# Performance work log

Measured on AMD Instinct MI355X. Metric: run time of the kernel, lower is better.

The kernel has to match this reference:

```python
import jax, jax.numpy as jnp
import numpy as np

B, N, E, H = 2, 2048, 1024, 16
D = E // H


def setup_inputs() -> dict:
    key = jax.random.key(0)
    ks = jax.random.split(key, 10)
    s = 0.02  # small init so softmax is well-conditioned
    return {
        "x": jax.random.normal(ks[0], (B, N, E), jnp.float32),
        "y": jax.random.normal(ks[1], (B, N, E), jnp.float32),
        # W stored as [in, out]; torch Linear computes x @ W_t.T + b, equivalent here.
        "Wq": jax.random.normal(ks[2], (E, E), jnp.float32) * s,
        "bq": jax.random.normal(ks[3], (E,), jnp.float32) * s,
        "Wk": jax.random.normal(ks[4], (E, E), jnp.float32) * s,
        "bk": jax.random.normal(ks[5], (E,), jnp.float32) * s,
        "Wv": jax.random.normal(ks[6], (E, E), jnp.float32) * s,
        "bv": jax.random.normal(ks[7], (E,), jnp.float32) * s,
        "Wo": jax.random.normal(ks[8], (E, E), jnp.float32) * s,
        "bo": jax.random.normal(ks[9], (E,), jnp.float32) * s,
    }


def _split_heads(t):
    # [b, n, (h d)] -> [b, h, n, d]
    b, n, e = t.shape
    return t.reshape(b, n, H, D).transpose(0, 2, 1, 3)


def reference(x, y, Wq, bq, Wk, bk, Wv, bv, Wo, bo):
    q = _split_heads(x @ Wq + bq)          # [b,h,n,d]
    k = _split_heads(y @ Wk + bk)
    v = _split_heads(y @ Wv + bv)
    energy = jnp.einsum('bhqd,bhkd->bhqk', q, k)            # [b,h,n,n]
    # Faithful quirk: softmax first, then divide by sqrt(emb_size).
    scaling = jnp.asarray(E, x.dtype) ** 0.5
    att = jax.nn.softmax(energy, axis=-1) / scaling
    out = jnp.einsum('bhqk,bhkd->bhqd', att, v)             # [b,h,n,d]
    out = out.transpose(0, 2, 1, 3).reshape(x.shape[0], x.shape[1], E)
    return out @ Wo + bo
```

## Files before the change

### kernel.cpp

```cpp
#include <hip/hip_runtime.h>
#include <stdint.h>

#define BATCH 2
#define SEQ   2048
#define EMB   1024
#define NH    16
#define HD    64
#define MROWS (BATCH*SEQ)
#define LOG2E 1.4426950408889634f

using bf16x8 = __attribute__((ext_vector_type(8))) short;
using f32x4  = __attribute__((ext_vector_type(4))) float;
using f32x16 = __attribute__((ext_vector_type(16))) float;

__device__ __forceinline__ unsigned short f2bf(float f) {
  __bf16 b = (__bf16)f;
  return __builtin_bit_cast(unsigned short, b);
}

__device__ __forceinline__ unsigned int cvtpk_bf16(float lo, float hi) {
  unsigned int w;
  asm("v_cvt_pk_bf16_f32 %0, %1, %2" : "=v"(w) : "v"(lo), "v"(hi));
  return w;
}

#if __has_builtin(__builtin_amdgcn_exp2f)
__device__ __forceinline__ float fast_exp2(float x) { return __builtin_amdgcn_exp2f(x); }
#else
__device__ __forceinline__ float fast_exp2(float x) {
  float r;
  asm("v_exp_f32 %0, %1\n\ts_nop 1" : "=v"(r) : "v"(x));
  return r;
}
#endif

__device__ __forceinline__ void swap32(unsigned int& a, unsigned int& b, int hi) {
#if __has_builtin(__builtin_amdgcn_permlane32_swap)
  (void)hi;
  typedef unsigned int u32x2_t __attribute__((ext_vector_type(2)));
  u32x2_t r = __builtin_amdgcn_permlane32_swap(a, b, false, false);
  a = r[0]; b = r[1];
#else
  const unsigned int ca = __shfl_xor(a, 32), cb = __shfl_xor(b, 32);
  const unsigned int na = hi ? cb : a;
  const unsigned int nb = hi ? b : ca;
  a = na; b = nb;
#endif
}

__device__ __forceinline__ float xadd32(float x, int hi) {
  unsigned int a = __builtin_bit_cast(unsigned int, x), b = a;
  swap32(a, b, hi);
  return __builtin_bit_cast(float, a) + __builtin_bit_cast(float, b);
}

__device__ __forceinline__ void async_load16(const void* g, void* l) {
  __builtin_amdgcn_global_load_lds(
      (__attribute__((address_space(1))) void*)g,
      (__attribute__((address_space(3))) void*)l,
      16, 0, 0);
}

__global__ __launch_bounds__(256) void prep_kernel(
    const float* __restrict__ x, const float* __restrict__ y,
    const float* __restrict__ Wq, const float* __restrict__ Wk,
    const float* __restrict__ Wv, const float* __restrict__ Wo,
    unsigned short* __restrict__ xb, unsigned short* __restrict__ yb,
    unsigned short* __restrict__ WtAll) {
  __shared__ unsigned short tile[64][65];
  const int lin = blockIdx.x;
  if (lin < 8192) {
    const float* in = (lin < 4096) ? x : y;
    unsigned short* out = (lin < 4096) ? xb : yb;
    const int i = (lin & 4095) * 256 + threadIdx.x;
    const float4 v = reinterpret_cast<const float4*>(in)[i];
    ushort4 o;
    o.x = f2bf(v.x); o.y = f2bf(v.y); o.z = f2bf(v.z); o.w = f2bf(v.w);
    reinterpret_cast<ushort4*>(out)[i] = o;
    return;
  }
  const int tw = lin - 8192;
  const int z = tw >> 8;
  const float* W = (z == 0) ? Wq : (z == 1) ? Wk : (z == 2) ? Wv : Wo;
  unsigned short* Wt = WtAll + (size_t)z * EMB * EMB;
  const int tc = threadIdx.x & 15;
  const int tr = threadIdx.x >> 4;
  const int n0 = ((tw >> 4) & 15) * 64, k0 = (tw & 15) * 64;
#pragma unroll
  for (int rr = 0; rr < 4; ++rr) {
    const int row = rr * 16 + tr;
    float4 v = *reinterpret_cast<const float4*>(W + (size_t)(k0 + row) * EMB + n0 + tc * 4);
    tile[tc * 4 + 0][row] = f2bf(v.x);
    tile[tc * 4 + 1][row] = f2bf(v.y);
    tile[tc * 4 + 2][row] = f2bf(v.z);
    tile[tc * 4 + 3][row] = f2bf(v.w);
  }
  __syncthreads();
#pragma unroll
  for (int rr = 0; rr < 4; ++rr) {
    const int row = rr * 16 + tr;
    ushort4 o;
    o.x = tile[row][tc * 4 + 0];
    o.y = tile[row][tc * 4 + 1];
    o.z = tile[row][tc * 4 + 2];
    o.w = tile[row][tc * 4 + 3];
    *reinterpret_cast<ushort4*>(Wt + (size_t)(n0 + row) * EMB + k0 + tc * 4) = o;
  }
}

#define BN 128
#define BK 32
#define NKS (EMB/BK)

template <int BMt>
__global__ __launch_bounds__(256, 3) void gemm_kernel(
    const unsigned short* __restrict__ xb,
    const unsigned short* __restrict__ yb,
    const unsigned short* __restrict__ attnb,
    const unsigned short* __restrict__ WtAll,
    const float* __restrict__ bq, const float* __restrict__ bk,
    const float* __restrict__ bv, const float* __restrict__ bo,
    unsigned short* __restrict__ Qb, unsigned short* __restrict__ Kb,
    unsigned short* __restrict__ Vt, float* __restrict__ dout,
    int phase) {
  __shared__ __align__(16) unsigned short As[3][BMt * BK];
  __shared__ __align__(16) unsigned short Bs[3][BN * BK];

  const int z = blockIdx.z;
  const unsigned short* A;
  const unsigned short* Bt;
  const float* bias;
  int mode;
  if (phase == 0) {
    A    = (z == 0) ? xb : yb;
    Bt   = WtAll + (size_t)z * EMB * EMB;
    bias = (z == 0) ? bq : (z == 1) ? bk : bv;
    mode = z;
  } else {
    A = attnb; Bt = WtAll + (size_t)3 * EMB * EMB; bias = bo; mode = 3;
  }

  const int tid = threadIdx.x;
  const int lane = tid & 63, wid = tid >> 6;
  constexpr int WC  = (BMt == 128) ? 2 : 4;
  constexpr int WCW = 128 / WC;
  constexpr int JN  = WCW / 16;
  const int wr = (BMt == 128) ? (wid >> 1) : 0;
  const int wc = (BMt == 128) ? (wid & 1) : wid;
  const int l15 = lane & 15, l4 = lane >> 4;
  const int m0 = blockIdx.y * BMt, n0 = blockIdx.x * BN;

  const int crow = tid >> 2;
  const int cslot = tid & 3;
  const int ssw = cslot ^ ((crow >> 1) & 3);
  const int rsw = (l15 >> 1) & 3;

  auto GSTAGE = [&](int b, int kt) {
    if constexpr (BMt == 128) {
#pragma unroll
      for (int it = 0; it < 2; ++it)
        async_load16(A + (size_t)(m0 + it * 64 + crow) * EMB + kt + ssw * 8,
                     (char*)As[b] + it * 4096 + wid * 1024);
    } else {
      async_load16(A + (size_t)(m0 + crow) * EMB + kt + ssw * 8,
                   (char*)As[b] + wid * 1024);
    }
#pragma unroll
    for (int it = 0; it < 2; ++it)
      async_load16(Bt + (size_t)(n0 + it * 64 + crow) * EMB + kt + ssw * 8,
                   (char*)Bs[b] + it * 4096 + wid * 1024);
  };

  GSTAGE(0, 0);
  GSTAGE(1, BK);

  f32x4 acc[4][JN] = {};

  int buf = 0, sb = 2;
  for (int s = 0; s < NKS; ++s) {
    __builtin_amdgcn_sched_barrier(0);
    if (s < NKS - 1) {
      if constexpr (BMt == 128) {
        asm volatile("s_waitcnt vmcnt(4)" ::: "memory");
      } else {
        asm volatile("s_waitcnt vmcnt(3)" ::: "memory");
      }
    } else {
      asm volatile("s_waitcnt vmcnt(0)" ::: "memory");
    }
    __builtin_amdgcn_s_barrier();
    __builtin_amdgcn_sched_barrier(0);

    if (s + 2 < NKS) { GSTAGE(sb, (s + 2) * BK); }

    bf16x8 af[4], bfr[JN];
#pragma unroll
    for (int i = 0; i < 4; ++i)
      af[i] = *reinterpret_cast<const bf16x8*>(
          (const char*)As[buf] + (wr * 64 + i * 16 + l15) * 64 + ((l4 ^ rsw) * 16));
#pragma unroll
    for (int j = 0; j < JN; ++j)
      bfr[j] = *reinterpret_cast<const bf16x8*>(
          (const char*)Bs[buf] + (wc * WCW + j * 16 + l15) * 64 + ((l4 ^ rsw) * 16));
#pragma unroll
    for (int i = 0; i < 4; ++i)
#pragma unroll
      for (int j = 0; j < JN; ++j)
        acc[i][j] = __builtin_amdgcn_mfma_f32_16x16x32_bf16(af[i], bfr[j], acc[i][j], 0, 0, 0);

    buf = (buf == 2) ? 0 : buf + 1;
    sb  = (sb  == 2) ? 0 : sb + 1;
  }

#pragma unroll
  for (int i = 0; i < 4; ++i) {
#pragma unroll
    for (int j = 0; j < JN; ++j) {
      const int col = n0 + wc * WCW + j * 16 + l15;
      const float bsv = bias[col];
#pragma unroll
      for (int r = 0; r < 4; ++r) {
        const int row = m0 + wr * 64 + i * 16 + l4 * 4 + r;
        const float v = acc[i][j][r] + bsv;
        if (mode == 3) {
          dout[(size_t)row * EMB + col] = v;
        } else {
          const int b = row >> 11, n = row & (SEQ - 1);
          const int h = col >> 6, d = col & (HD - 1);
          if (mode == 0)
            Qb[(((size_t)(b * NH + h)) * SEQ + n) * HD + d] = f2bf(v);
          else if (mode == 1)
            Kb[(((size_t)(b * NH + h)) * SEQ + n) * HD + d] = f2bf(v * LOG2E);
          else
            Vt[(((size_t)(b * NH + h)) * HD + d) * SEQ + n] = f2bf(v);
        }
      }
    }
  }
}

#define KVB 64
#define NT  (SEQ/KVB)

__global__ __launch_bounds__(256, 2) void flash_kernel(
    const unsigned short* __restrict__ Qb,
    const unsigned short* __restrict__ Kb,
    const unsigned short* __restrict__ Vt,
    unsigned short* __restrict__ attnb) {
  __shared__ __align__(16) char Ks[3][8192];
  __shared__ __align__(16) char Vs[3][8192];

  const int tid = threadIdx.x;
  const int lane = tid & 63, wid = tid >> 6;
  const int l31 = lane & 31, hi = lane >> 5;

  const int lin = blockIdx.x;
  const int swz = (lin & 7) * 64 + (lin >> 3);
  const int bh = swz >> 4;
  const int qt = swz & 15;
  const int bb = bh >> 4, hh = bh & 15;
  const int q0 = qt * 128 + wid * 32;

  const unsigned short* Qp = Qb + (size_t)bh * SEQ * HD;
  const unsigned short* Kp = Kb + (size_t)bh * SEQ * HD;
  const unsigned short* Vp = Vt + (size_t)bh * HD * SEQ;

  const int srow = tid >> 3;
  const int sslot = tid & 7;

  bf16x8 qf[4];
#pragma unroll
  for (int kt = 0; kt < 4; ++kt)
    qf[kt] = *reinterpret_cast<const bf16x8*>(Qp + (size_t)(q0 + l31) * HD + kt * 16 + hi * 8);

#define SWZ(r) (((r) & 7) ^ (((r) >> 3) & 7))
#define STAGE(b, kv)                                                          \
  {                                                                           \
    _Pragma("unroll")                                                         \
    for (int it = 0; it < 2; ++it) {                                          \
      const int r = it * 32 + srow;                                           \
      async_load16(Kp + (size_t)((kv) + r) * HD + ((sslot ^ SWZ(r)) * 8),     \
                   Ks[b] + it * 4096 + tid * 16);                             \
      async_load16(Vp + (size_t)r * SEQ + (kv) + ((sslot ^ SWZ(r)) * 8),      \
                   Vs[b] + it * 4096 + tid * 16);                             \
    }                                                                         \
  }

  STAGE(0, 0)
  STAGE(1, KVB)

  f32x16 accO[2] = {};
  float lp[8] = {0.f, 0.f, 0.f, 0.f, 0.f, 0.f, 0.f, 0.f};

  int buf = 0, sb = 2;
  for (int t = 0; t < NT; ++t) {
    __builtin_amdgcn_sched_barrier(0);
    if (t < NT - 1) {
      asm volatile("s_waitcnt vmcnt(4)" ::: "memory");
    } else {
      asm volatile("s_waitcnt vmcnt(0)" ::: "memory");
    }
    __builtin_amdgcn_s_barrier();
    __builtin_amdgcn_sched_barrier(0);

    if (t + 2 < NT) { STAGE(sb, (t + 2) * KVB) }

    bf16x8 kf[2][4];
#pragma unroll
    for (int t2 = 0; t2 < 2; ++t2)
#pragma unroll
      for (int kt = 0; kt < 4; ++kt) {
        const int key = t2 * 32 + l31;
        kf[t2][kt] = *reinterpret_cast<const bf16x8*>(
            Ks[buf] + key * 128 + (((kt * 2 + hi) ^ SWZ(key)) * 16));
      }
    bf16x8 vf[2][4];
#pragma unroll
    for (int dt = 0; dt < 2; ++dt)
#pragma unroll
      for (int kt = 0; kt < 4; ++kt) {
        const int d = dt * 32 + l31;
        vf[dt][kt] = *reinterpret_cast<const bf16x8*>(
            Vs[buf] + d * 128 + (((kt * 2 + hi) ^ SWZ(d)) * 16));
      }

    f32x16 sc[2] = {};
#pragma unroll
    for (int t2 = 0; t2 < 2; ++t2)
#pragma unroll
      for (int kt = 0; kt < 4; ++kt)
        sc[t2] = __builtin_amdgcn_mfma_f32_32x32x16_bf16(kf[t2][kt], qf[kt], sc[t2], 0, 0, 0);

#pragma unroll
    for (int t2 = 0; t2 < 2; ++t2)
#pragma unroll
      for (int r = 0; r < 16; ++r) {
        sc[t2][r] = fast_exp2(sc[t2][r]);
        lp[(t2 << 2) | (r & 3)] += sc[t2][r];
      }

    bf16x8 pf[4];
#pragma unroll
    for (int kt = 0; kt < 4; ++kt) {
      const int t2 = kt >> 1, g = (kt & 1) * 8;
      unsigned int Aw = cvtpk_bf16(sc[t2][g + 0], sc[t2][g + 1]);
      unsigned int Cw = cvtpk_bf16(sc[t2][g + 2], sc[t2][g + 3]);
      unsigned int Bw = cvtpk_bf16(sc[t2][g + 4], sc[t2][g + 5]);
      unsigned int Dw = cvtpk_bf16(sc[t2][g + 6], sc[t2][g + 7]);
      swap32(Aw, Bw, hi);
      swap32(Cw, Dw, hi);
      union { unsigned int u[4]; bf16x8 v; } cvt;
      cvt.u[0] = Aw; cvt.u[1] = Cw; cvt.u[2] = Bw; cvt.u[3] = Dw;
      pf[kt] = cvt.v;
    }

#pragma unroll
    for (int dt = 0; dt < 2; ++dt)
#pragma unroll
      for (int kt = 0; kt < 4; ++kt)
        accO[dt] = __builtin_amdgcn_mfma_f32_32x32x16_bf16(vf[dt][kt], pf[kt], accO[dt], 0, 0, 0);

    buf = (buf == 2) ? 0 : buf + 1;
    sb  = (sb  == 2) ? 0 : sb + 1;
  }
#undef STAGE
#undef SWZ

  const float ls = ((lp[0] + lp[1]) + (lp[2] + lp[3])) +
                   ((lp[4] + lp[5]) + (lp[6] + lp[7]));
  const float lI = xadd32(ls, hi);
  const float inv = 1.0f / (lI * 32.0f);
  const size_t obase = ((size_t)(bb * SEQ + q0 + l31)) * EMB + hh * HD;
#pragma unroll
  for (int dt = 0; dt < 2; ++dt)
#pragma unroll
    for (int rr = 0; rr < 4; ++rr) {
      ushort4 o;
      o.x = f2bf(accO[dt][rr * 4 + 0] * inv);
      o.y = f2bf(accO[dt][rr * 4 + 1] * inv);
      o.z = f2bf(accO[dt][rr * 4 + 2] * inv);
      o.w = f2bf(accO[dt][rr * 4 + 3] * inv);
      *reinterpret_cast<ushort4*>(attnb + obase + dt * 32 + 8 * rr + 4 * hi) = o;
    }
}

extern "C" void kernel_launch(void* const* d_in, const int* in_sizes, int n_in,
                              void* d_out, int out_size, void* d_ws, size_t ws_size,
                              hipStream_t stream) {
  (void)in_sizes; (void)n_in; (void)out_size;
  const float* x  = (const float*)d_in[0];
  const float* y  = (const float*)d_in[1];
  const float* Wq = (const float*)d_in[2];
  const float* bq = (const float*)d_in[3];
  const float* Wk = (const float*)d_in[4];
  const float* bk = (const float*)d_in[5];
  const float* Wv = (const float*)d_in[6];
  const float* bv = (const float*)d_in[7];
  const float* Wo = (const float*)d_in[8];
  const float* bo = (const float*)d_in[9];
  float* out = (float*)d_out;

  char* ws = (char*)d_ws;
  unsigned short* xb    = (unsigned short*)(ws + (size_t)(0u  << 20));
  unsigned short* yb    = (unsigned short*)(ws + (size_t)(8u  << 20));
  unsigned short* WtAll = (unsigned short*)(ws + (size_t)(16u << 20));
  unsigned short* Qb    = (unsigned short*)(ws + (size_t)(24u << 20));
  unsigned short* Kb    = (unsigned short*)(ws + (size_t)(32u << 20));
  unsigned short* Vt    = (unsigned short*)(ws + (size_t)(40u << 20));
  unsigned short* attnb = (unsigned short*)(ws + (size_t)(48u << 20));
  if (ws_size < ((size_t)56u << 20)) return;

  hipLaunchKernelGGL(prep_kernel, dim3(9216), dim3(256), 0, stream,
                     x, y, Wq, Wk, Wv, Wo, xb, yb, WtAll);
  hipLaunchKernelGGL((gemm_kernel<128>), dim3(EMB / BN, MROWS / 128, 3), dim3(256), 0, stream,
                     xb, yb, attnb, WtAll, bq, bk, bv, bo, Qb, Kb, Vt, out, 0);
  hipLaunchKernelGGL(flash_kernel, dim3(SEQ / 128 * BATCH * NH), dim3(256), 0, stream,
                     Qb, Kb, Vt, attnb);
  hipLaunchKernelGGL((gemm_kernel<64>), dim3(EMB / BN, MROWS / 64, 1), dim3(256), 0, stream,
                     xb, yb, attnb, WtAll, bq, bk, bv, bo, Qb, Kb, Vt, out, 1);
}
```

Before: 127.5 us.

## Split attention KV range across two blocks and merge partials in combine kernel

```diff
diff --git a/kernel.cpp b/kernel.cpp
--- a/kernel.cpp
+++ b/kernel.cpp
@@ -16,6 +16,10 @@
 __device__ __forceinline__ unsigned short f2bf(float f) {
   __bf16 b = (__bf16)f;
   return __builtin_bit_cast(unsigned short, b);
+}
+
+__device__ __forceinline__ float bf2f(unsigned short u) {
+  return __builtin_bit_cast(float, (unsigned int)u << 16);
 }
 
 __device__ __forceinline__ unsigned int cvtpk_bf16(float lo, float hi) {
@@ -240,13 +244,15 @@
 }
 
 #define KVB 64
-#define NT  (SEQ/KVB)
-
-__global__ __launch_bounds__(256, 2) void flash_kernel(
+#define NTH (SEQ/KVB/2)
+
+__global__ __launch_bounds__(256, 3) void flash_kernel(
     const unsigned short* __restrict__ Qb,
     const unsigned short* __restrict__ Kb,
     const unsigned short* __restrict__ Vt,
-    unsigned short* __restrict__ attnb) {
+    unsigned short* __restrict__ pA,
+    unsigned short* __restrict__ pB,
+    float* __restrict__ lP) {
   __shared__ __align__(16) char Ks[3][8192];
   __shared__ __align__(16) char Vs[3][8192];
 
@@ -255,6 +261,7 @@
   const int l31 = lane & 31, hi = lane >> 5;
 
   const int lin = blockIdx.x;
+  const int half = blockIdx.y;
   const int swz = (lin & 7) * 64 + (lin >> 3);
   const int bh = swz >> 4;
   const int qt = swz & 15;
@@ -262,8 +269,8 @@
   const int q0 = qt * 128 + wid * 32;
 
   const unsigned short* Qp = Qb + (size_t)bh * SEQ * HD;
-  const unsigned short* Kp = Kb + (size_t)bh * SEQ * HD;
-  const unsigned short* Vp = Vt + (size_t)bh * HD * SEQ;
+  const unsigned short* Kp = Kb + (size_t)bh * SEQ * HD + (size_t)half * (SEQ / 2) * HD;
+  const unsigned short* Vp = Vt + (size_t)bh * HD * SEQ + (size_t)half * (SEQ / 2);
 
   const int srow = tid >> 3;
   const int sslot = tid & 7;
@@ -293,9 +300,9 @@
   float lp[8] = {0.f, 0.f, 0.f, 0.f, 0.f, 0.f, 0.f, 0.f};
 
   int buf = 0, sb = 2;
-  for (int t = 0; t < NT; ++t) {
+  for (int t = 0; t < NTH; ++t) {
     __builtin_amdgcn_sched_barrier(0);
-    if (t < NT - 1) {
+    if (t < NTH - 1) {
       asm volatile("s_waitcnt vmcnt(4)" ::: "memory");
     } else {
       asm volatile("s_waitcnt vmcnt(0)" ::: "memory");
@@ -303,7 +310,7 @@
     __builtin_amdgcn_s_barrier();
     __builtin_amdgcn_sched_barrier(0);
 
-    if (t + 2 < NT) { STAGE(sb, (t + 2) * KVB) }
+    if (t + 2 < NTH) { STAGE(sb, (t + 2) * KVB) }
 
     bf16x8 kf[2][4];
 #pragma unroll
@@ -314,16 +321,6 @@
         kf[t2][kt] = *reinterpret_cast<const bf16x8*>(
             Ks[buf] + key * 128 + (((kt * 2 + hi) ^ SWZ(key)) * 16));
       }
-    bf16x8 vf[2][4];
-#pragma unroll
-    for (int dt = 0; dt < 2; ++dt)
-#pragma unroll
-      for (int kt = 0; kt < 4; ++kt) {
-        const int d = dt * 32 + l31;
-        vf[dt][kt] = *reinterpret_cast<const bf16x8*>(
-            Vs[buf] + d * 128 + (((kt * 2 + hi) ^ SWZ(d)) * 16));
-      }
-
     f32x16 sc[2] = {};
 #pragma unroll
     for (int t2 = 0; t2 < 2; ++t2)
@@ -354,6 +351,15 @@
       pf[kt] = cvt.v;
     }
 
+    bf16x8 vf[2][4];
+#pragma unroll
+    for (int dt = 0; dt < 2; ++dt)
+#pragma unroll
+      for (int kt = 0; kt < 4; ++kt) {
+        const int d = dt * 32 + l31;
+        vf[dt][kt] = *reinterpret_cast<const bf16x8*>(
+            Vs[buf] + d * 128 + (((kt * 2 + hi) ^ SWZ(d)) * 16));
+      }
 #pragma unroll
     for (int dt = 0; dt < 2; ++dt)
 #pragma unroll
@@ -369,19 +375,46 @@
   const float ls = ((lp[0] + lp[1]) + (lp[2] + lp[3])) +
                    ((lp[4] + lp[5]) + (lp[6] + lp[7]));
   const float lI = xadd32(ls, hi);
-  const float inv = 1.0f / (lI * 32.0f);
+  unsigned short* pOut = half ? pB : pA;
+  if (hi == 0) lP[(size_t)half * 32 * SEQ + bh * SEQ + q0 + l31] = lI;
   const size_t obase = ((size_t)(bb * SEQ + q0 + l31)) * EMB + hh * HD;
 #pragma unroll
   for (int dt = 0; dt < 2; ++dt)
 #pragma unroll
     for (int rr = 0; rr < 4; ++rr) {
       ushort4 o;
-      o.x = f2bf(accO[dt][rr * 4 + 0] * inv);
-      o.y = f2bf(accO[dt][rr * 4 + 1] * inv);
-      o.z = f2bf(accO[dt][rr * 4 + 2] * inv);
-      o.w = f2bf(accO[dt][rr * 4 + 3] * inv);
-      *reinterpret_cast<ushort4*>(attnb + obase + dt * 32 + 8 * rr + 4 * hi) = o;
-    }
+      o.x = f2bf(accO[dt][rr * 4 + 0]);
+      o.y = f2bf(accO[dt][rr * 4 + 1]);
+      o.z = f2bf(accO[dt][rr * 4 + 2]);
+      o.w = f2bf(accO[dt][rr * 4 + 3]);
+      *reinterpret_cast<ushort4*>(pOut + obase + dt * 32 + 8 * rr + 4 * hi) = o;
+    }
+}
+
+__global__ __launch_bounds__(256) void combine_kernel(
+    const unsigned short* __restrict__ pA, const unsigned short* __restrict__ pB,
+    const float* __restrict__ lP, unsigned short* __restrict__ attnb) {
+  const int idx = blockIdx.x * 256 + threadIdx.x;
+  const int row = idx >> 7;
+  const int c8  = idx & 127;
+  const int b = row >> 11, n = row & (SEQ - 1);
+  const int h = c8 >> 3;
+  const int bh = b * NH + h;
+  const float l1 = lP[(size_t)bh * SEQ + n];
+  const float l2 = lP[(size_t)32 * SEQ + (size_t)bh * SEQ + n];
+  const float inv = 1.0f / ((l1 + l2) * 32.0f);
+  const size_t off = (size_t)row * EMB + c8 * 8;
+  union { ushort4 u4[2]; unsigned short u[8]; } a, c;
+  a.u4[0] = *reinterpret_cast<const ushort4*>(pA + off);
+  a.u4[1] = *reinterpret_cast<const ushort4*>(pA + off + 4);
+  c.u4[0] = *reinterpret_cast<const ushort4*>(pB + off);
+  c.u4[1] = *reinterpret_cast<const ushort4*>(pB + off + 4);
+  union { ushort4 u4[2]; unsigned short u[8]; } o;
+#pragma unroll
+  for (int i = 0; i < 8; ++i)
+    o.u[i] = f2bf((bf2f(a.u[i]) + bf2f(c.u[i])) * inv);
+  *reinterpret_cast<ushort4*>(attnb + off) = o.u4[0];
+  *reinterpret_cast<ushort4*>(attnb + off + 4) = o.u4[1];
 }
 
 extern "C" void kernel_launch(void* const* d_in, const int* in_sizes, int n_in,
@@ -408,14 +441,19 @@
   unsigned short* Kb    = (unsigned short*)(ws + (size_t)(32u << 20));
   unsigned short* Vt    = (unsigned short*)(ws + (size_t)(40u << 20));
   unsigned short* attnb = (unsigned short*)(ws + (size_t)(48u << 20));
+  unsigned short* pA = xb;
+  unsigned short* pB = yb;
+  float* lP = (float*)(ws + (size_t)(16u << 20));
   if (ws_size < ((size_t)56u << 20)) return;
 
   hipLaunchKernelGGL(prep_kernel, dim3(9216), dim3(256), 0, stream,
                      x, y, Wq, Wk, Wv, Wo, xb, yb, WtAll);
   hipLaunchKernelGGL((gemm_kernel<128>), dim3(EMB / BN, MROWS / 128, 3), dim3(256), 0, stream,
                      xb, yb, attnb, WtAll, bq, bk, bv, bo, Qb, Kb, Vt, out, 0);
-  hipLaunchKernelGGL(flash_kernel, dim3(SEQ / 128 * BATCH * NH), dim3(256), 0, stream,
-                     Qb, Kb, Vt, attnb);
+  hipLaunchKernelGGL(flash_kernel, dim3(512, 2), dim3(256), 0, stream,
+                     Qb, Kb, Vt, pA, pB, lP);
+  hipLaunchKernelGGL(combine_kernel, dim3(2048), dim3(256), 0, stream,
+                     pA, pB, lP, attnb);
   hipLaunchKernelGGL((gemm_kernel<64>), dim3(EMB / BN, MROWS / 64, 1), dim3(256), 0, stream,
                      xb, yb, attnb, WtAll, bq, bk, bv, bo, Qb, Kb, Vt, out, 1);
 }
```

Measured after the change: 136.3 us. 6.9% more time.
